# Performance work log

Hardware: AMD Instinct MI355X
Metric: run time of the kernel (lower is better)

The kernel has to match this reference:

```python
import jax, jax.numpy as jnp
import numpy as np

S = 64.0
M = 0.5
EPS = 1e-07
NORM_EPS = 1e-12  # matches torch F.normalize default eps
B, D, C = 512, 512, 64000


def _l2_normalize(a, axis=-1):
    n = jnp.sqrt(jnp.sum(a * a, axis=axis, keepdims=True))
    return a / jnp.maximum(n, NORM_EPS)


def setup_inputs() -> dict:
    key = jax.random.key(0)
    kx, ky, kw = jax.random.split(key, 3)
    x = jax.random.normal(kx, (B, D), dtype=jnp.float32)
    y = jax.random.randint(ky, (B,), 0, C, dtype=jnp.int64)
    # kaiming_uniform-ish init: bound = sqrt(6 / fan_in)
    bound = np.sqrt(6.0 / D).astype(np.float32)
    W = jax.random.uniform(kw, (C, D), dtype=jnp.float32, minval=-bound, maxval=bound)
    return {"x": x, "y": y, "W": W}


def reference(x, y, W):
    # cosine similarities: [B, C]
    theta = _l2_normalize(x) @ _l2_normalize(W).T
    # target logit per row
    tgt = jnp.take_along_axis(theta, y[:, None], axis=1)[:, 0]  # [B]
    numerator = S * jnp.cos(jnp.arccos(jnp.clip(tgt, -1.0 + EPS, 1.0 - EPS)) + M)
    # sum of exp(s*theta) over non-target classes (mask out target column)
    is_tgt = jnp.arange(C, dtype=y.dtype)[None, :] == y[:, None]  # [B, C]
    excl_sum = jnp.sum(jnp.where(is_tgt, 0.0, jnp.exp(S * theta)), axis=1)  # [B]
    denominator = jnp.exp(numerator) + excl_sum
    return -jnp.mean(numerator - jnp.log(denominator))
```

## Files before the change

kernel.cpp:

```cpp
#include <hip/hip_runtime.h>


#define B_N 512
#define D_N 512
#define C_N 64000
#define S_SCALE 64.0f
#define MARGIN 0.5f
#define EPS_C 1e-7f

typedef unsigned short ushort_t;
typedef __attribute__((ext_vector_type(8))) short short8;
typedef __attribute__((ext_vector_type(4))) float floatx4;

__device__ __forceinline__ ushort_t f2bf(float f) {
    unsigned int u = __float_as_uint(f);
    u += 0x7fffu + ((u >> 16) & 1u);
    return (ushort_t)(u >> 16);
}

__global__ void norm_rows_kernel(const float* __restrict__ src,
                                 ushort_t* __restrict__ dst, int nrows) {
    int row  = blockIdx.x * 4 + (threadIdx.x >> 6);
    int lane = threadIdx.x & 63;
    if (row >= nrows) return;
    const float4* p = (const float4*)(src + (size_t)row * D_N);
    float4 v0 = p[lane * 2];
    float4 v1 = p[lane * 2 + 1];
    float ss = v0.x*v0.x + v0.y*v0.y + v0.z*v0.z + v0.w*v0.w
             + v1.x*v1.x + v1.y*v1.y + v1.z*v1.z + v1.w*v1.w;
#pragma unroll
    for (int off = 32; off > 0; off >>= 1) ss += __shfl_xor(ss, off);
    float scale = 1.0f / fmaxf(sqrtf(ss), 1e-12f);
    uint4 o;
    o.x = (unsigned)f2bf(v0.x*scale) | ((unsigned)f2bf(v0.y*scale) << 16);
    o.y = (unsigned)f2bf(v0.z*scale) | ((unsigned)f2bf(v0.w*scale) << 16);
    o.z = (unsigned)f2bf(v1.x*scale) | ((unsigned)f2bf(v1.y*scale) << 16);
    o.w = (unsigned)f2bf(v1.z*scale) | ((unsigned)f2bf(v1.w*scale) << 16);
    *((uint4*)(dst + (size_t)row * D_N + lane * 8)) = o;
}

__device__ __forceinline__ void g2lds16(const ushort_t* g, ushort_t* l) {
    __builtin_amdgcn_global_load_lds(
        (const __attribute__((address_space(1))) void*)g,
        (__attribute__((address_space(3))) void*)l, 16, 0, 0);
}

__global__ void gemm_arcface_kernel(const ushort_t* __restrict__ A,
                                    const ushort_t* __restrict__ Bm,
                                    const int* __restrict__ y,
                                    float* __restrict__ rowsum,
                                    float* __restrict__ tgt) {
    __shared__ ushort_t sA[128 * 32];
    __shared__ ushort_t sB[128 * 32];
    __shared__ float rowacc[128];

    int t    = threadIdx.x;
    int lane = t & 63;
    int w    = t >> 6;
    int wr   = w >> 1, wc = w & 1;
    int rm0  = blockIdx.y * 128;
    int cn0  = blockIdx.x * 128;

    if (t < 128) rowacc[t] = 0.0f;

    floatx4 acc[4][4];
#pragma unroll
    for (int i = 0; i < 4; i++)
#pragma unroll
        for (int j = 0; j < 4; j++) acc[i][j] = (floatx4){0.f, 0.f, 0.f, 0.f};

    const ushort_t* gA0 = A  + (size_t)(rm0 + (t >> 2)) * D_N + (t & 3) * 8;
    const ushort_t* gB0 = Bm + (size_t)(cn0 + (t >> 2)) * D_N + (t & 3) * 8;

    int lq = lane >> 4;
    int lc = lane & 15;
    int fragA_off = (wr * 64 + lc) * 32 + lq * 8;
    int fragB_off = (wc * 64 + lc) * 32 + lq * 8;

    for (int kk = 0; kk < D_N; kk += 32) {
        g2lds16(gA0 + kk,            sA + t * 8);
        g2lds16(gA0 + 64 * D_N + kk, sA + (t + 256) * 8);
        g2lds16(gB0 + kk,            sB + t * 8);
        g2lds16(gB0 + 64 * D_N + kk, sB + (t + 256) * 8);
        __syncthreads();

        short8 af[4], bf[4];
#pragma unroll
        for (int tm = 0; tm < 4; tm++)
            af[tm] = *(const short8*)(sA + fragA_off + tm * 512);
#pragma unroll
        for (int tn = 0; tn < 4; tn++)
            bf[tn] = *(const short8*)(sB + fragB_off + tn * 512);
#pragma unroll
        for (int tm = 0; tm < 4; tm++)
#pragma unroll
            for (int tn = 0; tn < 4; tn++)
                acc[tm][tn] = __builtin_amdgcn_mfma_f32_16x16x32_bf16(
                    af[tm], bf[tn], acc[tm][tn], 0, 0, 0);
        __syncthreads();
    }

#pragma unroll
    for (int tm = 0; tm < 4; tm++) {
#pragma unroll
        for (int r = 0; r < 4; r++) {
            int lrow = wr * 64 + tm * 16 + lq * 4 + r;
            int grow = rm0 + lrow;
            int yv   = y[grow];
            float esum = 0.0f;
#pragma unroll
            for (int tn = 0; tn < 4; tn++) {
                int gcol = cn0 + wc * 64 + tn * 16 + lc;
                float theta = acc[tm][tn][r];
                if (gcol == yv) {
                    tgt[grow] = theta;
                } else {
                    esum += __expf(S_SCALE * theta);
                }
            }
#pragma unroll
            for (int off = 1; off < 16; off <<= 1) esum += __shfl_xor(esum, off);
            if (lc == 0) atomicAdd(&rowacc[lrow], esum);
        }
    }
    __syncthreads();
    if (t < 128) atomicAdd(&rowsum[rm0 + t], rowacc[t]);
}

__global__ void finalize_kernel(const float* __restrict__ rowsum,
                                const float* __restrict__ tgt,
                                float* __restrict__ out) {
    __shared__ float red[256];
    int t = threadIdx.x;
    float s = 0.0f;
    for (int r = t; r < B_N; r += 256) {
        float tv = tgt[r];
        tv = fminf(fmaxf(tv, -1.0f + EPS_C), 1.0f - EPS_C);
        float num = S_SCALE * cosf(acosf(tv) + MARGIN);
        float den = expf(num) + rowsum[r];
        s += num - logf(den);
    }
    red[t] = s;
    __syncthreads();
    for (int o = 128; o > 0; o >>= 1) {
        if (t < o) red[t] += red[t + o];
        __syncthreads();
    }
    if (t == 0) out[0] = -red[0] / (float)B_N;
}

extern "C" void kernel_launch(void* const* d_in, const int* in_sizes, int n_in,
                              void* d_out, int out_size, void* d_ws, size_t ws_size,
                              hipStream_t stream) {
    const float* x = (const float*)d_in[0];
    const int*   y = (const int*)d_in[1];
    const float* W = (const float*)d_in[2];
    float* out = (float*)d_out;

    char* ws = (char*)d_ws;
    ushort_t* xn = (ushort_t*)ws;
    ushort_t* Wn = (ushort_t*)(ws + 524288);
    float* rowsum = (float*)(ws + 524288 + (size_t)C_N * D_N * 2);
    float* tgt    = rowsum + B_N;

    hipMemsetAsync(rowsum, 0, B_N * sizeof(float), stream);
    norm_rows_kernel<<<B_N / 4, 256, 0, stream>>>(x, xn, B_N);
    norm_rows_kernel<<<C_N / 4, 256, 0, stream>>>(W, Wn, C_N);
    dim3 grid(C_N / 128, B_N / 128);
    gemm_arcface_kernel<<<grid, 256, 0, stream>>>(xn, Wn, y, rowsum, tgt);
    finalize_kernel<<<1, 256, 0, stream>>>(rowsum, tgt, out);
}
```

Before: 273.7 us.

## Double-buffer GEMM LDS loads, fuse prep kernels, swap grid order

Adds a two-stage LDS double buffer so the next K-slice's global-to-LDS loads are issued while the current slice's MFMAs run, keeping one barrier per iteration. The two normalization launches and the memset are merged into a single prep kernel with coalesced float4 loads. The GEMM grid is transposed so that the four row-blocks sharing a W column tile are scheduled next to each other, which should help L2 reuse of W. LDS use doubles, which may lower occupancy.

Result: faster. 256.0 us (-6.5%).

```diff
diff --git a/kernel.cpp b/kernel.cpp
--- a/kernel.cpp
+++ b/kernel.cpp
@@ -18,25 +18,46 @@
     return (ushort_t)(u >> 16);
 }
 
-__global__ void norm_rows_kernel(const float* __restrict__ src,
-                                 ushort_t* __restrict__ dst, int nrows) {
-    int row  = blockIdx.x * 4 + (threadIdx.x >> 6);
-    int lane = threadIdx.x & 63;
-    if (row >= nrows) return;
-    const float4* p = (const float4*)(src + (size_t)row * D_N);
-    float4 v0 = p[lane * 2];
-    float4 v1 = p[lane * 2 + 1];
+__global__ void prep_kernel(const float* __restrict__ W,
+                            const float* __restrict__ x,
+                            ushort_t* __restrict__ Wn,
+                            ushort_t* __restrict__ xn,
+                            float* __restrict__ rowsum) {
+    int b = blockIdx.x;
+    int t = threadIdx.x;
+    if (b == 16128) {
+        rowsum[t] = 0.0f;
+        rowsum[t + 256] = 0.0f;
+        return;
+    }
+    const float* src;
+    ushort_t* dst;
+    int row;
+    if (b < 16000) {
+        row = b * 4 + (t >> 6);
+        src = W + (size_t)row * D_N;
+        dst = Wn + (size_t)row * D_N;
+    } else {
+        row = (b - 16000) * 4 + (t >> 6);
+        src = x + (size_t)row * D_N;
+        dst = xn + (size_t)row * D_N;
+    }
+    int lane = t & 63;
+    const float4* p = (const float4*)src;
+    float4 v0 = p[lane];
+    float4 v1 = p[lane + 64];
     float ss = v0.x*v0.x + v0.y*v0.y + v0.z*v0.z + v0.w*v0.w
              + v1.x*v1.x + v1.y*v1.y + v1.z*v1.z + v1.w*v1.w;
 #pragma unroll
     for (int off = 32; off > 0; off >>= 1) ss += __shfl_xor(ss, off);
-    float scale = 1.0f / fmaxf(sqrtf(ss), 1e-12f);
-    uint4 o;
-    o.x = (unsigned)f2bf(v0.x*scale) | ((unsigned)f2bf(v0.y*scale) << 16);
-    o.y = (unsigned)f2bf(v0.z*scale) | ((unsigned)f2bf(v0.w*scale) << 16);
-    o.z = (unsigned)f2bf(v1.x*scale) | ((unsigned)f2bf(v1.y*scale) << 16);
-    o.w = (unsigned)f2bf(v1.z*scale) | ((unsigned)f2bf(v1.w*scale) << 16);
-    *((uint4*)(dst + (size_t)row * D_N + lane * 8)) = o;
+    float sc = 1.0f / fmaxf(sqrtf(ss), 1e-12f);
+    uint2 o0, o1;
+    o0.x = (unsigned)f2bf(v0.x*sc) | ((unsigned)f2bf(v0.y*sc) << 16);
+    o0.y = (unsigned)f2bf(v0.z*sc) | ((unsigned)f2bf(v0.w*sc) << 16);
+    o1.x = (unsigned)f2bf(v1.x*sc) | ((unsigned)f2bf(v1.y*sc) << 16);
+    o1.y = (unsigned)f2bf(v1.z*sc) | ((unsigned)f2bf(v1.w*sc) << 16);
+    *(uint2*)(dst + lane * 4)       = o0;
+    *(uint2*)(dst + 256 + lane * 4) = o1;
 }
 
 __device__ __forceinline__ void g2lds16(const ushort_t* g, ushort_t* l) {
@@ -50,16 +71,16 @@
                                     const int* __restrict__ y,
                                     float* __restrict__ rowsum,
                                     float* __restrict__ tgt) {
-    __shared__ ushort_t sA[128 * 32];
-    __shared__ ushort_t sB[128 * 32];
+    __shared__ ushort_t sA[2 * 128 * 32];
+    __shared__ ushort_t sB[2 * 128 * 32];
     __shared__ float rowacc[128];
 
     int t    = threadIdx.x;
     int lane = t & 63;
     int w    = t >> 6;
     int wr   = w >> 1, wc = w & 1;
-    int rm0  = blockIdx.y * 128;
-    int cn0  = blockIdx.x * 128;
+    int rm0  = blockIdx.x * 128;
+    int cn0  = blockIdx.y * 128;
 
     if (t < 128) rowacc[t] = 0.0f;
 
@@ -77,20 +98,30 @@
     int fragA_off = (wr * 64 + lc) * 32 + lq * 8;
     int fragB_off = (wc * 64 + lc) * 32 + lq * 8;
 
-    for (int kk = 0; kk < D_N; kk += 32) {
-        g2lds16(gA0 + kk,            sA + t * 8);
-        g2lds16(gA0 + 64 * D_N + kk, sA + (t + 256) * 8);
-        g2lds16(gB0 + kk,            sB + t * 8);
-        g2lds16(gB0 + 64 * D_N + kk, sB + (t + 256) * 8);
-        __syncthreads();
+    g2lds16(gA0,            sA + t * 8);
+    g2lds16(gA0 + 64 * D_N, sA + (t + 256) * 8);
+    g2lds16(gB0,            sB + t * 8);
+    g2lds16(gB0 + 64 * D_N, sB + (t + 256) * 8);
+    __syncthreads();
+
+    for (int k = 0; k < 16; ++k) {
+        int cur = (k & 1) * 4096;
+        if (k < 15) {
+            int nxt = ((k + 1) & 1) * 4096;
+            int kk  = (k + 1) * 32;
+            g2lds16(gA0 + kk,            sA + nxt + t * 8);
+            g2lds16(gA0 + 64 * D_N + kk, sA + nxt + (t + 256) * 8);
+            g2lds16(gB0 + kk,            sB + nxt + t * 8);
+            g2lds16(gB0 + 64 * D_N + kk, sB + nxt + (t + 256) * 8);
+        }
 
         short8 af[4], bf[4];
 #pragma unroll
         for (int tm = 0; tm < 4; tm++)
-            af[tm] = *(const short8*)(sA + fragA_off + tm * 512);
+            af[tm] = *(const short8*)(sA + cur + fragA_off + tm * 512);
 #pragma unroll
         for (int tn = 0; tn < 4; tn++)
-            bf[tn] = *(const short8*)(sB + fragB_off + tn * 512);
+            bf[tn] = *(const short8*)(sB + cur + fragB_off + tn * 512);
 #pragma unroll
         for (int tm = 0; tm < 4; tm++)
 #pragma unroll
@@ -163,10 +194,8 @@
     float* rowsum = (float*)(ws + 524288 + (size_t)C_N * D_N * 2);
     float* tgt    = rowsum + B_N;
 
-    hipMemsetAsync(rowsum, 0, B_N * sizeof(float), stream);
-    norm_rows_kernel<<<B_N / 4, 256, 0, stream>>>(x, xn, B_N);
-    norm_rows_kernel<<<C_N / 4, 256, 0, stream>>>(W, Wn, C_N);
-    dim3 grid(C_N / 128, B_N / 128);
+    prep_kernel<<<16129, 256, 0, stream>>>(W, x, Wn, xn, rowsum);
+    dim3 grid(4, C_N / 128);
     gemm_arcface_kernel<<<grid, 256, 0, stream>>>(xn, Wn, y, rowsum, tgt);
     finalize_kernel<<<1, 256, 0, stream>>>(rowsum, tgt, out);
 }
```
